# Kernel optimization log

Measured on AMD Instinct MI355X. Metric: run time of the kernel, lower is better.

Reference implementation:

```python
import jax, jax.numpy as jnp
import numpy as np
from jax import lax

B, N, S, K = 8, 8192, 1024, 32
R2 = 0.2 ** 2
EPS = 1e-5


def _gather(p, idx):
    # p: [B, N, C]; idx: [B, ...] int -> p[b, idx[b]]
    bidx = jnp.arange(p.shape[0]).reshape((p.shape[0],) + (1,) * (idx.ndim - 1))
    return p[bidx, idx]


def _fps(xyz):
    # farthest point sampling; deterministic start at index 0 (torch version uses randint)
    def step(carry, _):
        dist, far = carry
        c = _gather(xyz, far[:, None])            # [B,1,3]
        d = jnp.sum((xyz - c) ** 2, -1)           # [B,N]
        dist = jnp.minimum(dist, d)
        return (dist, jnp.argmax(dist, -1).astype(jnp.int32)), far
    init = (jnp.full(xyz.shape[:2], 1e10, xyz.dtype), jnp.zeros((xyz.shape[0],), jnp.int32))
    _, idx = lax.scan(step, init, None, length=S)
    return idx.T                                   # [B,S]


def _ball_query(xyz, new_xyz):
    # squared dists [B,S,N]
    sq = (jnp.sum(new_xyz ** 2, -1)[:, :, None] + jnp.sum(xyz ** 2, -1)[:, None, :]
          - 2.0 * jnp.einsum('bsc,bnc->bsn', new_xyz, xyz))
    gi = jnp.where(sq > R2, N, jnp.arange(N, dtype=jnp.int32))
    # K smallest indices within radius == K largest of (N - gi); equivalent to sort()[:, :, :K]
    vals, _ = lax.top_k(N - gi, K)
    gi = N - vals                                  # [B,S,K]
    first = gi[:, :, :1]
    return jnp.where(gi == N, first, gi)


def _forward(xyz, points, params):
    xyz = xyz.transpose(0, 2, 1)                   # [B,N,3]
    points = points.transpose(0, 2, 1)             # [B,N,C]
    fps_idx = _fps(xyz)                            # [B,S]
    new_xyz = _gather(xyz, fps_idx)                # [B,S,3]
    gi = _ball_query(xyz, new_xyz)                 # [B,S,K]
    g_xyz = _gather(xyz, gi) - new_xyz[:, :, None, :]            # [B,S,K,3]
    g_pts = jnp.concatenate([_gather(points, gi), g_xyz], -1)    # [B,S,K,C+3]
    x = g_pts.transpose(0, 3, 2, 1)                # [B,C+3,K,S]
    for w, b, g, be in params:
        x = jnp.einsum('oc,bcks->boks', w, x) + b[None, :, None, None]
        m = jnp.mean(x, axis=(0, 2, 3), keepdims=True)
        v = jnp.mean((x - m) ** 2, axis=(0, 2, 3), keepdims=True)  # biased var (BN train mode)
        x = jax.nn.relu(g[None, :, None, None] * (x - m) / jnp.sqrt(v + EPS) + be[None, :, None, None])
    return new_xyz.transpose(0, 2, 1), jnp.max(x, axis=2)          # [B,3,S], [B,128,S]


def setup_inputs() -> dict:
    key = jax.random.key(0)
    ks = jax.random.split(key, 8)
    chans = [(67, 64), (64, 64), (64, 128)]
    inp = {
        'xyz': jax.random.normal(ks[0], (B, 3, N), jnp.float32),
        'points': jax.random.normal(ks[1], (B, 64, N), jnp.float32),
    }
    for i, (ci, co) in enumerate(chans):
        kw = jax.random.fold_in(ks[2], i)
        inp[f'w{i}'] = jax.random.normal(kw, (co, ci), jnp.float32) * 0.1
        inp[f'b{i}'] = jnp.zeros((co,), jnp.float32)
        inp[f'g{i}'] = jnp.ones((co,), jnp.float32)
        inp[f'be{i}'] = jnp.zeros((co,), jnp.float32)
    return inp


def reference(xyz, points, w0, b0, g0, be0, w1, b1, g1, be1, w2, b2, g2, be2):
    params = [(w0, b0, g0, be0), (w1, b1, g1, be1), (w2, b2, g2, be2)]
    return _forward(xyz, points, params)
```

## Files before the change

### kernel.cpp

```cpp
#include <hip/hip_runtime.h>

typedef unsigned short ushort_t;
typedef unsigned int uint_t;
typedef unsigned long long u64_t;
typedef unsigned short us8 __attribute__((ext_vector_type(8)));

constexpr int B_ = 8, N_ = 8192, S_ = 1024, K_ = 32;
constexpr int M_ = B_ * S_ * K_;
constexpr float R2_ = 0.04f;
constexpr float EPS_ = 1e-5f;

__device__ __forceinline__ float bf2f(ushort_t u) {
    union { uint_t i; float f; } v; v.i = ((uint_t)u) << 16; return v.f;
}
__device__ __forceinline__ ushort_t f2bf(float f) {
    union { float f; uint_t i; } v; v.f = f;
    uint_t i = v.i;
    uint_t r = (i + 0x7FFFu + ((i >> 16) & 1u)) >> 16;
    return (ushort_t)r;
}

template<int C> __device__ __forceinline__ float dmaxf(float v) {
    int o = __builtin_amdgcn_mov_dpp(__float_as_int(v), C, 0xf, 0xf, true);
    return fmaxf(v, __int_as_float(o));
}

__global__ __launch_bounds__(1024, 4)
void fps_kernel(const float* __restrict__ xyz, float* __restrict__ nxyz,
                float* __restrict__ out0) {
    constexpr int T = 1024, P = N_ / T;
    const int b = blockIdx.x, t = threadIdx.x;
    const int lane = t & 63, w = t >> 6;
    const float* X = xyz + (size_t)b * 3 * N_;

    __shared__ float4 sxyz[N_];
    __shared__ float rv[16];
    __shared__ int sfar;
    __shared__ int sidx[S_];

#pragma unroll
    for (int i = 0; i < P; ++i) {
        int n = t + i * T;
        sxyz[n] = make_float4(X[n], X[N_ + n], X[2 * N_ + n], 0.0f);
    }
    if (t == 0) sidx[0] = 0;
    __syncthreads();

    float px[P], py[P], pz[P], dist[P];
#pragma unroll
    for (int i = 0; i < P; ++i) {
        int j = (i + t) & (P - 1);
        float4 v = sxyz[t * P + j];
        px[j] = v.x; py[j] = v.y; pz[j] = v.z;
        dist[j] = 1e10f;
    }
    float4 cc = sxyz[0];
    float cx = cc.x, cy = cc.y, cz = cc.z;

    for (int s = 0; s < S_; ++s) {
#pragma unroll
        for (int i = 0; i < P; ++i) {
            float dx = __fsub_rn(px[i], cx);
            float dy = __fsub_rn(py[i], cy);
            float dz = __fsub_rn(pz[i], cz);
            float d = __fadd_rn(__fadd_rn(__fmul_rn(dx, dx), __fmul_rn(dy, dy)), __fmul_rn(dz, dz));
            dist[i] = fminf(dist[i], d);
        }
        float a0 = fmaxf(dist[0], dist[4]);
        float a1 = fmaxf(dist[1], dist[5]);
        float a2 = fmaxf(dist[2], dist[6]);
        float a3 = fmaxf(dist[3], dist[7]);
        float lmax = fmaxf(fmaxf(a0, a1), fmaxf(a2, a3));
        float m = lmax;
        m = dmaxf<0x111>(m);
        m = dmaxf<0x112>(m);
        m = dmaxf<0x114>(m);
        m = dmaxf<0x118>(m);
        m = dmaxf<0x142>(m);
        m = dmaxf<0x143>(m);
        if (lane == 63) rv[w] = m;
        __syncthreads();

        float kv0 = rv[lane & 15];
        float kv = kv0;
        kv = dmaxf<0x121>(kv);
        kv = dmaxf<0x122>(kv);
        kv = dmaxf<0x124>(kv);
        kv = dmaxf<0x128>(kv);
        float gmax = kv;
        u64_t wm = __ballot(kv0 == gmax);
        int first_w = __builtin_ctzll(wm);

        if (w == first_w) {
            u64_t lm = __ballot(lmax == gmax);
            int L = __builtin_ctzll(lm);
            if (lane == L) {
                int fi = 0;
#pragma unroll
                for (int i = P - 1; i >= 0; --i)
                    if (dist[i] == gmax) fi = i;
                int nf = t * P + fi;
                sfar = nf;
                if (s + 1 < S_) sidx[s + 1] = nf;
            }
        }
        __syncthreads();
        int nf = sfar;
        float4 c = sxyz[nf];
        cx = c.x; cy = c.y; cz = c.z;
    }

    __syncthreads();
    {
        int s = t;
        int idx = sidx[s];
        float4 c = sxyz[idx];
        size_t base = ((size_t)b * S_ + s) * 3;
        nxyz[base + 0] = c.x; nxyz[base + 1] = c.y; nxyz[base + 2] = c.z;
        out0[((size_t)b * 3 + 0) * S_ + s] = c.x;
        out0[((size_t)b * 3 + 1) * S_ + s] = c.y;
        out0[((size_t)b * 3 + 2) * S_ + s] = c.z;
    }
}

__global__ __launch_bounds__(256)
void ballq_kernel(const float* __restrict__ xyz, const float* __restrict__ nxyz,
                  int* __restrict__ gi) {
    int wid = (blockIdx.x * 256 + threadIdx.x) >> 6;
    int lane = threadIdx.x & 63;
    if (wid >= B_ * S_) return;
    int b = wid / S_;
    const float* X = xyz + (size_t)b * 3 * N_;
    float nx = nxyz[(size_t)wid * 3 + 0];
    float ny = nxyz[(size_t)wid * 3 + 1];
    float nz = nxyz[(size_t)wid * 3 + 2];
    float snew = __fadd_rn(__fadd_rn(__fmul_rn(nx, nx), __fmul_rn(ny, ny)), __fmul_rn(nz, nz));
    int cnt = 0; int firstn = 0;
    int* out = gi + (size_t)wid * K_;
    for (int c0 = 0; c0 < N_; c0 += 64) {
        int n = c0 + lane;
        float xx = X[n], xy = X[N_ + n], xz = X[2 * N_ + n];
        float sxn = __fadd_rn(__fadd_rn(__fmul_rn(xx, xx), __fmul_rn(xy, xy)), __fmul_rn(xz, xz));
        float dot = __fadd_rn(__fadd_rn(__fmul_rn(nx, xx), __fmul_rn(ny, xy)), __fmul_rn(nz, xz));
        float sq = __fsub_rn(__fadd_rn(snew, sxn), __fmul_rn(2.0f, dot));
        bool inr = !(sq > R2_);
        unsigned long long mask = __ballot(inr);
        if (cnt == 0 && mask) firstn = c0 + __builtin_ctzll(mask);
        int rank = __popcll(mask & ((1ull << lane) - 1ull));
        if (inr && cnt + rank < K_) out[cnt + rank] = n;
        cnt += (int)__popcll(mask);
        if (cnt >= K_) break;
    }
    if (cnt < K_ && lane >= cnt && lane < K_) out[lane] = firstn;
}

__global__ __launch_bounds__(256)
void transpose_pts(const float* __restrict__ pts, ushort_t* __restrict__ ptT) {
    __shared__ ushort_t tile[64][66];
    int b = blockIdx.y; int n0 = blockIdx.x * 64;
    int tc = threadIdx.x & 63;
    int tr = threadIdx.x >> 6;
    const float* src = pts + (size_t)b * 64 * N_;
#pragma unroll
    for (int i = 0; i < 16; ++i) {
        int c = i * 4 + tr;
        tile[c][tc] = f2bf(src[(size_t)c * N_ + n0 + tc]);
    }
    __syncthreads();
#pragma unroll
    for (int i = 0; i < 16; ++i) {
        int nr = i * 4 + tr;
        ptT[((size_t)b * N_ + n0 + nr) * 64 + tc] = tile[tc][nr];
    }
}

__global__ void wt_kernel(const float* __restrict__ w0, const float* __restrict__ w1,
                          const float* __restrict__ w2, float* __restrict__ wt,
                          float* __restrict__ stats) {
    int l = blockIdx.x;
    if (l == 0) {
        for (int i = threadIdx.x; i < 768; i += 256) stats[i] = 0.0f;
    }
    const float* w = l == 0 ? w0 : (l == 1 ? w1 : w2);
    int CI = (l == 0) ? 67 : 64;
    int CO = (l == 2) ? 128 : 64;
    float* dst = wt + (l == 0 ? 0 : (l == 1 ? 67 * 64 : 67 * 64 + 64 * 64));
    for (int i = threadIdx.x; i < CI * CO; i += 256) {
        int c = i / CO, o = i % CO;
        dst[c * CO + o] = w[o * CI + c];
    }
}

__global__ __launch_bounds__(256)
void layer1_kernel(const ushort_t* __restrict__ ptT,
                   const float* __restrict__ xyz,
                   const float* __restrict__ nxyz,
                   const int* __restrict__ gi,
                   const float* __restrict__ WT,
                   const float* __restrict__ bias,
                   ushort_t* __restrict__ y,
                   float* __restrict__ sums) {
    constexpr int RP = 72;
    __shared__ ushort_t sb[256 * RP];
    __shared__ float ps[128], pq[128];
    int tid = threadIdx.x;
    int m = blockIdx.x * 256 + tid;
    float acc[64];
#pragma unroll
    for (int o = 0; o < 64; ++o) acc[o] = bias[o];

    int idx = gi[m];
    int b = m >> 15;
    const ushort_t* row = ptT + ((size_t)b * N_ + idx) * 64;
#pragma unroll
    for (int c8 = 0; c8 < 8; ++c8) {
        us8 v = *reinterpret_cast<const us8*>(row + c8 * 8);
#pragma unroll
        for (int j = 0; j < 8; ++j) {
            int c = c8 * 8 + j;
            float h = bf2f(v[j]);
            const float* wr = WT + (size_t)c * 64;
#pragma unroll
            for (int o = 0; o < 64; ++o) acc[o] = fmaf(h, wr[o], acc[o]);
        }
    }
    int s = (m >> 5) & (S_ - 1);
    const float* X = xyz + (size_t)b * 3 * N_;
    const float* nx = nxyz + ((size_t)(b * S_ + s)) * 3;
#pragma unroll
    for (int j = 0; j < 3; ++j) {
        float h = X[(size_t)j * N_ + idx] - nx[j];
        const float* wr = WT + (size_t)(64 + j) * 64;
#pragma unroll
        for (int o = 0; o < 64; ++o) acc[o] = fmaf(h, wr[o], acc[o]);
    }
    ushort_t* yr = y + (size_t)m * 64;
#pragma unroll
    for (int v8 = 0; v8 < 8; ++v8) {
        us8 wv;
#pragma unroll
        for (int j = 0; j < 8; ++j) wv[j] = f2bf(acc[v8 * 8 + j]);
        *reinterpret_cast<us8*>(yr + v8 * 8) = wv;
        *reinterpret_cast<us8*>(sb + tid * RP + v8 * 8) = wv;
    }
    __syncthreads();
    if (tid < 128) {
        int c = tid & 63, half = tid >> 6;
        float sv = 0.0f, qv = 0.0f;
        int r0 = half * 128;
        for (int r = 0; r < 128; ++r) {
            float v = bf2f(sb[(r0 + r) * RP + c]);
            sv += v; qv = fmaf(v, v, qv);
        }
        ps[tid] = sv; pq[tid] = qv;
    }
    __syncthreads();
    if (tid < 64) {
        atomicAdd(&sums[tid], ps[tid] + ps[tid + 64]);
        atomicAdd(&sums[128 + tid], pq[tid] + pq[tid + 64]);
    }
}

__global__ __launch_bounds__(256, 8)
void layer32_kernel(const ushort_t* __restrict__ xin,
                    const float* __restrict__ WT,
                    const float* __restrict__ bias,
                    const float* __restrict__ abuf,
                    ushort_t* __restrict__ y,
                    int COtot,
                    float* __restrict__ sums) {
    constexpr int RP = 40;
    __shared__ ushort_t sb[256 * RP];
    __shared__ float ps[64], pq[64];
    int tid = threadIdx.x;
    int m = blockIdx.x * 256 + tid;
    int os = blockIdx.y * 32;
    float acc[32];
#pragma unroll
    for (int o = 0; o < 32; ++o) acc[o] = bias[os + o];

    const ushort_t* row = xin + (size_t)m * 64;
#pragma unroll
    for (int c8 = 0; c8 < 8; ++c8) {
        us8 v = *reinterpret_cast<const us8*>(row + c8 * 8);
#pragma unroll
        for (int j = 0; j < 8; ++j) {
            int c = c8 * 8 + j;
            float h = fmaxf(fmaf(abuf[c], bf2f(v[j]), abuf[128 + c]), 0.0f);
            const float* wr = WT + (size_t)c * COtot + os;
#pragma unroll
            for (int o = 0; o < 32; ++o) acc[o] = fmaf(h, wr[o], acc[o]);
        }
    }
    ushort_t* yr = y + (size_t)m * COtot + os;
#pragma unroll
    for (int v8 = 0; v8 < 4; ++v8) {
        us8 wv;
#pragma unroll
        for (int j = 0; j < 8; ++j) wv[j] = f2bf(acc[v8 * 8 + j]);
        *reinterpret_cast<us8*>(yr + v8 * 8) = wv;
        *reinterpret_cast<us8*>(sb + tid * RP + v8 * 8) = wv;
    }
    __syncthreads();
    if (tid < 64) {
        int c = tid & 31, half = tid >> 5;
        float sv = 0.0f, qv = 0.0f;
        int r0 = half * 128;
        for (int r = 0; r < 128; ++r) {
            float v = bf2f(sb[(r0 + r) * RP + c]);
            sv += v; qv = fmaf(v, v, qv);
        }
        ps[tid] = sv; pq[tid] = qv;
    }
    __syncthreads();
    if (tid < 32) {
        int cg = os + tid;
        atomicAdd(&sums[cg], ps[tid] + ps[tid + 32]);
        atomicAdd(&sums[128 + cg], pq[tid] + pq[tid + 32]);
    }
}

__global__ void finalize_kernel(const float* __restrict__ sums, const float* __restrict__ g,
                                const float* __restrict__ be, float* __restrict__ ab, int CO) {
    int c = threadIdx.x;
    if (c < CO) {
        float mean = sums[c] * (1.0f / (float)M_);
        float var = sums[128 + c] * (1.0f / (float)M_) - mean * mean;
        float a = g[c] / sqrtf(var + EPS_);
        ab[c] = a;
        ab[128 + c] = be[c] - mean * a;
    }
}

__global__ __launch_bounds__(256)
void final_max(const ushort_t* __restrict__ x3, const float* __restrict__ ab,
               float* __restrict__ out1) {
    int t = threadIdx.x;
    int gw = blockIdx.x * 4 + (t >> 6);
    if (gw >= B_ * S_) return;
    int lane = t & 63;
    int b = gw / S_, s = gw % S_;
    int c0 = lane * 2;
    float a0 = ab[c0], k0 = ab[128 + c0];
    float a1 = ab[c0 + 1], k1 = ab[128 + c0 + 1];
    const ushort_t* base = x3 + (size_t)gw * K_ * 128;
    float m0 = -1e30f, m1 = -1e30f;
#pragma unroll 8
    for (int k = 0; k < K_; ++k) {
        uint_t v = *reinterpret_cast<const uint_t*>(base + k * 128 + c0);
        float f0 = fmaf(bf2f((ushort_t)(v & 0xffff)), a0, k0);
        float f1 = fmaf(bf2f((ushort_t)(v >> 16)), a1, k1);
        m0 = fmaxf(m0, f0); m1 = fmaxf(m1, f1);
    }
    out1[((size_t)b * 128 + c0) * S_ + s] = fmaxf(m0, 0.0f);
    out1[((size_t)b * 128 + c0 + 1) * S_ + s] = fmaxf(m1, 0.0f);
}

extern "C" void kernel_launch(void* const* d_in, const int* in_sizes, int n_in,
                              void* d_out, int out_size, void* d_ws, size_t ws_size,
                              hipStream_t stream) {
    const float* xyz = (const float*)d_in[0];
    const float* pts = (const float*)d_in[1];
    const float* w0 = (const float*)d_in[2];
    const float* b0 = (const float*)d_in[3];
    const float* g0 = (const float*)d_in[4];
    const float* be0 = (const float*)d_in[5];
    const float* w1 = (const float*)d_in[6];
    const float* b1 = (const float*)d_in[7];
    const float* g1 = (const float*)d_in[8];
    const float* be1 = (const float*)d_in[9];
    const float* w2 = (const float*)d_in[10];
    const float* b2 = (const float*)d_in[11];
    const float* g2 = (const float*)d_in[12];
    const float* be2 = (const float*)d_in[13];

    float* out0 = (float*)d_out;
    float* out1 = out0 + (size_t)B_ * 3 * S_;

    char* ws = (char*)d_ws;
    float*    nxyz  = (float*)(ws + 32768);
    int*      gi    = (int*)(ws + 131072);
    float*    stats = (float*)(ws + 1179648);
    float*    ab    = (float*)(ws + 1182720);
    float*    wt    = (float*)(ws + 1185792);
    ushort_t* ptT   = (ushort_t*)(ws + 2097152);
    ushort_t* xA    = (ushort_t*)(ws + 10485760);
    ushort_t* xB    = (ushort_t*)(ws + 77594624);

    wt_kernel<<<3, 256, 0, stream>>>(w0, w1, w2, wt, stats);
    transpose_pts<<<dim3(N_ / 64, B_), 256, 0, stream>>>(pts, ptT);
    fps_kernel<<<B_, 1024, 0, stream>>>(xyz, nxyz, out0);
    ballq_kernel<<<(B_ * S_) / 4, 256, 0, stream>>>(xyz, nxyz, gi);

    layer1_kernel<<<M_ / 256, 256, 0, stream>>>(ptT, xyz, nxyz, gi, wt, b0, xA, stats + 0);
    finalize_kernel<<<1, 128, 0, stream>>>(stats + 0, g0, be0, ab + 0, 64);

    layer32_kernel<<<dim3(M_ / 256, 2), 256, 0, stream>>>(
        xA, wt + 67 * 64, b1, ab + 0, xB, 64, stats + 256);
    finalize_kernel<<<1, 128, 0, stream>>>(stats + 256, g1, be1, ab + 256, 64);

    layer32_kernel<<<dim3(M_ / 256, 4), 256, 0, stream>>>(
        xB, wt + 67 * 64 + 64 * 64, b2, ab + 256, xA, 128, stats + 512);
    finalize_kernel<<<1, 128, 0, stream>>>(stats + 512, g2, be2, ab + 512, 128);

    final_max<<<(B_ * S_) / 4, 256, 0, stream>>>(xA, ab + 512, out1);
}
```

Baseline: 1.214 ms.

## Fuse prep kernels into FPS launch and fold BN finalize into consumers

Merges the weight-transpose, stats-zeroing and point-transpose kernels into the FPS launch as extra blocks, so they run alongside the 8 long-running FPS blocks on otherwise idle CUs. It also removes the three finalize_kernel launches by having each consuming kernel recompute the BN scale and shift into shared memory. This cuts launch count and serialization, at the cost of a redundant per-block stats computation and a larger shared allocation for every fused block.

```diff
diff --git a/kernel.cpp b/kernel.cpp
--- a/kernel.cpp
+++ b/kernel.cpp
@@ -25,18 +25,61 @@
     return fmaxf(v, __int_as_float(o));
 }
 
-__global__ __launch_bounds__(1024, 4)
-void fps_kernel(const float* __restrict__ xyz, float* __restrict__ nxyz,
-                float* __restrict__ out0) {
+__global__ __launch_bounds__(1024)
+void fps_fused(const float* __restrict__ xyz, const float* __restrict__ pts,
+               const float* __restrict__ w0, const float* __restrict__ w1,
+               const float* __restrict__ w2,
+               float* __restrict__ nxyz, float* __restrict__ out0,
+               ushort_t* __restrict__ ptT, float* __restrict__ wt,
+               float* __restrict__ stats) {
+    __shared__ __align__(16) char smem[131072 + 4096 + 64 + 16];
+    const int bx = blockIdx.x, t = threadIdx.x;
+
+    if (bx >= 8) {
+        if (bx == 264) {
+            if (t < 768) stats[t] = 0.0f;
+#pragma unroll
+            for (int l = 0; l < 3; ++l) {
+                const float* w = l == 0 ? w0 : (l == 1 ? w1 : w2);
+                int CI = (l == 0) ? 67 : 64;
+                int CO = (l == 2) ? 128 : 64;
+                float* dst = wt + (l == 0 ? 0 : (l == 1 ? 67 * 64 : 67 * 64 + 64 * 64));
+                for (int i = t; i < CI * CO; i += 1024) {
+                    int c = i / CO, o = i % CO;
+                    dst[c * CO + o] = w[o * CI + c];
+                }
+            }
+            return;
+        }
+        int g = t >> 8, lt = t & 255;
+        int tau = (bx - 8) * 4 + g;
+        int b = tau >> 7, n0 = (tau & 127) * 64;
+        int tc = lt & 63, tr = lt >> 6;
+        ushort_t* tile = (ushort_t*)(smem + g * 8448);
+        const float* src = pts + (size_t)b * 64 * N_;
+#pragma unroll
+        for (int i = 0; i < 16; ++i) {
+            int c = i * 4 + tr;
+            tile[c * 66 + tc] = f2bf(src[(size_t)c * N_ + n0 + tc]);
+        }
+        __syncthreads();
+#pragma unroll
+        for (int i = 0; i < 16; ++i) {
+            int nr = i * 4 + tr;
+            ptT[((size_t)b * N_ + n0 + nr) * 64 + tc] = tile[tc * 66 + nr];
+        }
+        return;
+    }
+
     constexpr int T = 1024, P = N_ / T;
-    const int b = blockIdx.x, t = threadIdx.x;
+    const int b = bx;
     const int lane = t & 63, w = t >> 6;
     const float* X = xyz + (size_t)b * 3 * N_;
 
-    __shared__ float4 sxyz[N_];
-    __shared__ float rv[16];
-    __shared__ int sfar;
-    __shared__ int sidx[S_];
+    float4* sxyz = (float4*)smem;
+    int*    sidx = (int*)(smem + 131072);
+    float*  rv   = (float*)(smem + 131072 + 4096);
+    int*    sfar = (int*)(smem + 131072 + 4096 + 64);
 
 #pragma unroll
     for (int i = 0; i < P; ++i) {
@@ -100,12 +143,12 @@
                 for (int i = P - 1; i >= 0; --i)
                     if (dist[i] == gmax) fi = i;
                 int nf = t * P + fi;
-                sfar = nf;
+                *sfar = nf;
                 if (s + 1 < S_) sidx[s + 1] = nf;
             }
         }
         __syncthreads();
-        int nf = sfar;
+        int nf = *sfar;
         float4 c = sxyz[nf];
         cx = c.x; cy = c.y; cz = c.z;
     }
@@ -155,43 +198,6 @@
 }
 
 __global__ __launch_bounds__(256)
-void transpose_pts(const float* __restrict__ pts, ushort_t* __restrict__ ptT) {
-    __shared__ ushort_t tile[64][66];
-    int b = blockIdx.y; int n0 = blockIdx.x * 64;
-    int tc = threadIdx.x & 63;
-    int tr = threadIdx.x >> 6;
-    const float* src = pts + (size_t)b * 64 * N_;
-#pragma unroll
-    for (int i = 0; i < 16; ++i) {
-        int c = i * 4 + tr;
-        tile[c][tc] = f2bf(src[(size_t)c * N_ + n0 + tc]);
-    }
-    __syncthreads();
-#pragma unroll
-    for (int i = 0; i < 16; ++i) {
-        int nr = i * 4 + tr;
-        ptT[((size_t)b * N_ + n0 + nr) * 64 + tc] = tile[tc][nr];
-    }
-}
-
-__global__ void wt_kernel(const float* __restrict__ w0, const float* __restrict__ w1,
-                          const float* __restrict__ w2, float* __restrict__ wt,
-                          float* __restrict__ stats) {
-    int l = blockIdx.x;
-    if (l == 0) {
-        for (int i = threadIdx.x; i < 768; i += 256) stats[i] = 0.0f;
-    }
-    const float* w = l == 0 ? w0 : (l == 1 ? w1 : w2);
-    int CI = (l == 0) ? 67 : 64;
-    int CO = (l == 2) ? 128 : 64;
-    float* dst = wt + (l == 0 ? 0 : (l == 1 ? 67 * 64 : 67 * 64 + 64 * 64));
-    for (int i = threadIdx.x; i < CI * CO; i += 256) {
-        int c = i / CO, o = i % CO;
-        dst[c * CO + o] = w[o * CI + c];
-    }
-}
-
-__global__ __launch_bounds__(256)
 void layer1_kernel(const ushort_t* __restrict__ ptT,
                    const float* __restrict__ xyz,
                    const float* __restrict__ nxyz,
@@ -265,14 +271,26 @@
 void layer32_kernel(const ushort_t* __restrict__ xin,
                     const float* __restrict__ WT,
                     const float* __restrict__ bias,
-                    const float* __restrict__ abuf,
+                    const float* __restrict__ sums_in,
+                    const float* __restrict__ g,
+                    const float* __restrict__ be,
                     ushort_t* __restrict__ y,
                     int COtot,
                     float* __restrict__ sums) {
     constexpr int RP = 40;
     __shared__ ushort_t sb[256 * RP];
     __shared__ float ps[64], pq[64];
+    __shared__ float s_a[64], s_sh[64];
     int tid = threadIdx.x;
+    if (tid < 64) {
+        float mean = sums_in[tid] * (1.0f / (float)M_);
+        float var = sums_in[128 + tid] * (1.0f / (float)M_) - mean * mean;
+        float a = g[tid] / sqrtf(var + EPS_);
+        s_a[tid] = a;
+        s_sh[tid] = be[tid] - mean * a;
+    }
+    __syncthreads();
+
     int m = blockIdx.x * 256 + tid;
     int os = blockIdx.y * 32;
     float acc[32];
@@ -286,7 +304,7 @@
 #pragma unroll
         for (int j = 0; j < 8; ++j) {
             int c = c8 * 8 + j;
-            float h = fmaxf(fmaf(abuf[c], bf2f(v[j]), abuf[128 + c]), 0.0f);
+            float h = fmaxf(fmaf(s_a[c], bf2f(v[j]), s_sh[c]), 0.0f);
             const float* wr = WT + (size_t)c * COtot + os;
 #pragma unroll
             for (int o = 0; o < 32; ++o) acc[o] = fmaf(h, wr[o], acc[o]);
@@ -320,29 +338,27 @@
     }
 }
 
-__global__ void finalize_kernel(const float* __restrict__ sums, const float* __restrict__ g,
-                                const float* __restrict__ be, float* __restrict__ ab, int CO) {
-    int c = threadIdx.x;
-    if (c < CO) {
-        float mean = sums[c] * (1.0f / (float)M_);
-        float var = sums[128 + c] * (1.0f / (float)M_) - mean * mean;
-        float a = g[c] / sqrtf(var + EPS_);
-        ab[c] = a;
-        ab[128 + c] = be[c] - mean * a;
-    }
-}
-
 __global__ __launch_bounds__(256)
-void final_max(const ushort_t* __restrict__ x3, const float* __restrict__ ab,
+void final_max(const ushort_t* __restrict__ x3, const float* __restrict__ sums,
+               const float* __restrict__ g, const float* __restrict__ be,
                float* __restrict__ out1) {
+    __shared__ float s_a[128], s_sh[128];
     int t = threadIdx.x;
+    if (t < 128) {
+        float mean = sums[t] * (1.0f / (float)M_);
+        float var = sums[128 + t] * (1.0f / (float)M_) - mean * mean;
+        float a = g[t] / sqrtf(var + EPS_);
+        s_a[t] = a;
+        s_sh[t] = be[t] - mean * a;
+    }
+    __syncthreads();
     int gw = blockIdx.x * 4 + (t >> 6);
     if (gw >= B_ * S_) return;
     int lane = t & 63;
     int b = gw / S_, s = gw % S_;
     int c0 = lane * 2;
-    float a0 = ab[c0], k0 = ab[128 + c0];
-    float a1 = ab[c0 + 1], k1 = ab[128 + c0 + 1];
+    float a0 = s_a[c0], k0 = s_sh[c0];
+    float a1 = s_a[c0 + 1], k1 = s_sh[c0 + 1];
     const ushort_t* base = x3 + (size_t)gw * K_ * 128;
     float m0 = -1e30f, m1 = -1e30f;
 #pragma unroll 8
@@ -381,27 +397,21 @@
     float*    nxyz  = (float*)(ws + 32768);
     int*      gi    = (int*)(ws + 131072);
     float*    stats = (float*)(ws + 1179648);
-    float*    ab    = (float*)(ws + 1182720);
     float*    wt    = (float*)(ws + 1185792);
     ushort_t* ptT   = (ushort_t*)(ws + 2097152);
     ushort_t* xA    = (ushort_t*)(ws + 10485760);
     ushort_t* xB    = (ushort_t*)(ws + 77594624);
 
-    wt_kernel<<<3, 256, 0, stream>>>(w0, w1, w2, wt, stats);
-    transpose_pts<<<dim3(N_ / 64, B_), 256, 0, stream>>>(pts, ptT);
-    fps_kernel<<<B_, 1024, 0, stream>>>(xyz, nxyz, out0);
+    fps_fused<<<265, 1024, 0, stream>>>(xyz, pts, w0, w1, w2, nxyz, out0, ptT, wt, stats);
     ballq_kernel<<<(B_ * S_) / 4, 256, 0, stream>>>(xyz, nxyz, gi);
 
     layer1_kernel<<<M_ / 256, 256, 0, stream>>>(ptT, xyz, nxyz, gi, wt, b0, xA, stats + 0);
-    finalize_kernel<<<1, 128, 0, stream>>>(stats + 0, g0, be0, ab + 0, 64);
 
     layer32_kernel<<<dim3(M_ / 256, 2), 256, 0, stream>>>(
-        xA, wt + 67 * 64, b1, ab + 0, xB, 64, stats + 256);
-    finalize_kernel<<<1, 128, 0, stream>>>(stats + 256, g1, be1, ab + 256, 64);
+        xA, wt + 67 * 64, b1, stats + 0, g0, be0, xB, 64, stats + 256);
 
     layer32_kernel<<<dim3(M_ / 256, 4), 256, 0, stream>>>(
-        xB, wt + 67 * 64 + 64 * 64, b2, ab + 256, xA, 128, stats + 512);
-    finalize_kernel<<<1, 128, 0, stream>>>(stats + 512, g2, be2, ab + 512, 128);
-
-    final_max<<<(B_ * S_) / 4, 256, 0, stream>>>(xA, ab + 512, out1);
-}
+        xB, wt + 67 * 64 + 64 * 64, b2, stats + 256, g1, be1, xA, 128, stats + 512);
+
+    final_max<<<(B_ * S_) / 4, 256, 0, stream>>>(xA, stats + 512, g2, be2, out1);
+}
```

Result: no change. 1.208 ms (-0.5%).
